# Kernel tuning notes

Measured on AMD Instinct MI355X. Metric: run time of the kernel, lower is better.

## Reference

```python
import jax, jax.numpy as jnp
import numpy as np

T, B, N = 1000, 64, 512
DT = 0.01
EL, VR, TR, TINF = -0.07, -0.07, -0.06, -0.05
A_VAL = 2.6239240169525146
A1_VAL = -0.015625353902578354
A2_VAL = -1.0590057373046875
B_VAL = 12.77495288848877
G_VAL = 45.24007797241211
K1, K2 = 200.0, 20.0
R1, R2 = 0.3858567178249359, -1.1421641111373901
C = 1.0


def setup_inputs() -> dict:
    key = jax.random.key(0)
    x = jax.random.normal(key, (T, B, N), dtype=jnp.float32)
    linear = jnp.ones((1, N), jnp.float32)
    a = jnp.full((1, N), A_VAL, jnp.float32)
    A1 = jnp.full((1, N), A1_VAL * C, jnp.float32)
    A2 = jnp.full((1, N), A2_VAL * C, jnp.float32)
    return {"x": x, "linear": linear, "a": a, "A1": A1, "A2": A2}


def _spike(v):
    # Heaviside step (forward of SurrGradSpike)
    return (v > 0).astype(v.dtype)


def reference(x, linear, a, A1, A2):
    G = G_VAL * C

    def step(state, xt):
        V, i1, i2, Thr = state
        i1 = i1 - K1 * i1 * DT
        i2 = i2 - K2 * i2 * DT
        V = V + DT * (linear * xt + i1 + i2 - G * (V - EL)) / C
        Thr = Thr + DT * (a * (V - EL) - B_VAL * (Thr - TINF))
        spk = _spike(V - Thr)
        i1 = (1.0 - spk) * i1 + spk * (R1 * i1 + A1)
        i2 = (1.0 - spk) * i2 + spk * (R2 * i2 + A2)
        Thr = (1.0 - spk) * Thr + spk * jnp.maximum(Thr, TR)
        V = (1.0 - spk) * V + spk * VR
        return (V, i1, i2, Thr), spk

    Bd, Nd = x.shape[1], x.shape[2]
    init = (
        jnp.full((Bd, Nd), EL, x.dtype),   # V
        jnp.zeros((Bd, Nd), x.dtype),      # i1
        jnp.zeros((Bd, Nd), x.dtype),      # i2
        jnp.full((Bd, Nd), TINF, x.dtype), # Thr
    )
    _, spikes = jax.lax.scan(step, init, x)
    return spikes  # [T, B, N] (original returns np.array of per-step spikes)
```

## Files before the change

kernel.cpp:

```cpp
#include <hip/hip_runtime.h>


#define T_STEPS 1000
#define B_DIM 64
#define N_DIM 512
#define BN (B_DIM * N_DIM)

#define K_CHUNK 20
#define NCHUNK (T_STEPS / K_CHUNK)
#define NBUF 8

#define C_DT   0.01f
#define C_EL   (-0.07f)
#define C_VR   (-0.07f)
#define C_TR   (-0.06f)
#define C_TINF (-0.05f)
#define C_B    12.77495288848877f
#define C_G    45.24007797241211f
#define C_K1   200.0f
#define C_K2   20.0f
#define C_R1   0.3858567178249359f
#define C_R2   (-1.1421641111373901f)

typedef const __attribute__((address_space(1))) void* gp_t;
typedef __attribute__((address_space(3))) void* lp_t;
typedef __attribute__((address_space(3))) float* lpf_t;

__device__ __forceinline__ float mn_step(float xt, float lin, float av,
                                         float A1v, float A2v,
                                         float& V, float& i1, float& i2,
                                         float& Thr)
{
#pragma clang fp contract(off)
    i1 = i1 - (C_K1 * i1) * C_DT;
    i2 = i2 - (C_K2 * i2) * C_DT;
    float p  = lin * xt;
    float q  = p + i1;
    float r  = q + i2;
    float e  = V - C_EL;
    float g  = C_G * e;
    float s  = r - g;
    float d  = C_DT * s;
    V = V + d;
    float e2 = V - C_EL;
    float u  = av * e2;
    float w  = Thr - C_TINF;
    float bw = C_B * w;
    float s2 = u - bw;
    float d2 = C_DT * s2;
    Thr = Thr + d2;
    float diff = V - Thr;
    bool  sb   = diff > 0.0f;
    float spk  = sb ? 1.0f : 0.0f;
    float i1r = (C_R1 * i1) + A1v;
    float i2r = (C_R2 * i2) + A2v;
    i1  = sb ? i1r : i1;
    i2  = sb ? i2r : i2;
    float tm = fmaxf(Thr, C_TR);
    Thr = sb ? tm : Thr;
    V   = sb ? C_VR : V;
    return spk;
}

__global__ __launch_bounds__(128) void mn_neuron_kernel(
    const float* __restrict__ x, const float* __restrict__ linear,
    const float* __restrict__ a, const float* __restrict__ A1,
    const float* __restrict__ A2, float* __restrict__ out)
{
#pragma clang fp contract(off)
    __shared__ float lds[NBUF][K_CHUNK][64];

    const int lane = threadIdx.x & 63;
    const int wid  = threadIdx.x >> 6;
    const int blk  = blockIdx.x;

    if (wid == 1) {
        const float* pl = x + (size_t)(lane >> 4) * BN
                            + (size_t)blk * 64 + (size_t)(lane & 15) * 4;

        auto issue_chunk = [&](int ch) {
            const float* pc = pl + (size_t)(ch * K_CHUNK) * BN;
            float* dst = &lds[ch & (NBUF - 1)][0][0];
#pragma unroll
            for (int s = 0; s < K_CHUNK / 4; ++s) {
                __builtin_amdgcn_global_load_lds(
                    (gp_t)(pc + (size_t)(s * 4) * BN),
                    (lp_t)(dst + s * 4 * 64), 16, 0, 0);
            }
        };

        for (int ch = 0; ch < NBUF - 1; ++ch) issue_chunk(ch);
        asm volatile("s_waitcnt vmcnt(30)" ::: "memory");
        __builtin_amdgcn_s_barrier();

        for (int c = 0; c <= NCHUNK - NBUF; ++c) {
            issue_chunk(c + NBUF - 1);
            asm volatile("s_waitcnt vmcnt(30)" ::: "memory");
            __builtin_amdgcn_s_barrier();
        }
        asm volatile("s_waitcnt vmcnt(25)" ::: "memory");
        __builtin_amdgcn_s_barrier();
        asm volatile("s_waitcnt vmcnt(20)" ::: "memory");
        __builtin_amdgcn_s_barrier();
        asm volatile("s_waitcnt vmcnt(15)" ::: "memory");
        __builtin_amdgcn_s_barrier();
        asm volatile("s_waitcnt vmcnt(10)" ::: "memory");
        __builtin_amdgcn_s_barrier();
        asm volatile("s_waitcnt vmcnt(5)" ::: "memory");
        __builtin_amdgcn_s_barrier();
        asm volatile("s_waitcnt vmcnt(0)" ::: "memory");
        __builtin_amdgcn_s_barrier();
        __builtin_amdgcn_s_barrier();
    } else {
        const int idx = blk * 64 + lane;
        const int n   = idx & (N_DIM - 1);

        const float lin = linear[n];
        const float av  = a[n];
        const float A1v = A1[n];
        const float A2v = A2[n];

        float V   = C_EL;
        float i1  = 0.0f;
        float i2  = 0.0f;
        float Thr = C_TINF;

        float* op = out + idx;

        __builtin_amdgcn_s_barrier();

        for (int c = 0; c < NCHUNK; ++c) {
            lpf_t lptr = (lpf_t)&lds[c & (NBUF - 1)][0][lane];

            float xv[K_CHUNK];
            asm volatile(
                "ds_read_b32 %0,  %20 offset:0\n\t"
                "ds_read_b32 %1,  %20 offset:256\n\t"
                "ds_read_b32 %2,  %20 offset:512\n\t"
                "ds_read_b32 %3,  %20 offset:768\n\t"
                "ds_read_b32 %4,  %20 offset:1024\n\t"
                "ds_read_b32 %5,  %20 offset:1280\n\t"
                "ds_read_b32 %6,  %20 offset:1536\n\t"
                "ds_read_b32 %7,  %20 offset:1792\n\t"
                "ds_read_b32 %8,  %20 offset:2048\n\t"
                "ds_read_b32 %9,  %20 offset:2304\n\t"
                "ds_read_b32 %10, %20 offset:2560\n\t"
                "ds_read_b32 %11, %20 offset:2816\n\t"
                "ds_read_b32 %12, %20 offset:3072\n\t"
                "ds_read_b32 %13, %20 offset:3328\n\t"
                "ds_read_b32 %14, %20 offset:3584\n\t"
                "ds_read_b32 %15, %20 offset:3840\n\t"
                "ds_read_b32 %16, %20 offset:4096\n\t"
                "ds_read_b32 %17, %20 offset:4352\n\t"
                "ds_read_b32 %18, %20 offset:4608\n\t"
                "ds_read_b32 %19, %20 offset:4864\n\t"
                "s_waitcnt lgkmcnt(0)"
                : "=&v"(xv[0]),  "=&v"(xv[1]),  "=&v"(xv[2]),  "=&v"(xv[3]),
                  "=&v"(xv[4]),  "=&v"(xv[5]),  "=&v"(xv[6]),  "=&v"(xv[7]),
                  "=&v"(xv[8]),  "=&v"(xv[9]),  "=&v"(xv[10]), "=&v"(xv[11]),
                  "=&v"(xv[12]), "=&v"(xv[13]), "=&v"(xv[14]), "=&v"(xv[15]),
                  "=&v"(xv[16]), "=&v"(xv[17]), "=&v"(xv[18]), "=&v"(xv[19])
                : "v"(lptr));

            __builtin_amdgcn_s_barrier();

#pragma unroll
            for (int j = 0; j < K_CHUNK; ++j) {
                float spk = mn_step(xv[j], lin, av, A1v, A2v, V, i1, i2, Thr);
                __builtin_nontemporal_store(spk, op);
                op += BN;
            }
        }
    }
}

extern "C" void kernel_launch(void* const* d_in, const int* in_sizes, int n_in,
                              void* d_out, int out_size, void* d_ws, size_t ws_size,
                              hipStream_t stream) {
    const float* x      = (const float*)d_in[0];
    const float* linear = (const float*)d_in[1];
    const float* a      = (const float*)d_in[2];
    const float* A1     = (const float*)d_in[3];
    const float* A2     = (const float*)d_in[4];
    float* out = (float*)d_out;

    mn_neuron_kernel<<<BN / 64, 128, 0, stream>>>(x, linear, a, A1, A2, out);
}
```

Baseline: 246.1 us.

## Speculatively precompute both spike branches to shorten per-step dependency chain

Restructures the neuron recurrence so that each step's reset-dependent quantities (i1/i2 decay, G*(V-EL), B*(Thr-TINF), clamped threshold) are computed for both the spike and no-spike outcomes ahead of time. The actual spike bit then only selects between the precomputed values. This is meant to take the reset selects and decay arithmetic off the serial critical path of the time loop, in exchange for extra ALU work and registers per step.

```diff
diff --git a/kernel.cpp b/kernel.cpp
--- a/kernel.cpp
+++ b/kernel.cpp
@@ -26,42 +26,6 @@
 typedef __attribute__((address_space(3))) void* lp_t;
 typedef __attribute__((address_space(3))) float* lpf_t;
 
-__device__ __forceinline__ float mn_step(float xt, float lin, float av,
-                                         float A1v, float A2v,
-                                         float& V, float& i1, float& i2,
-                                         float& Thr)
-{
-#pragma clang fp contract(off)
-    i1 = i1 - (C_K1 * i1) * C_DT;
-    i2 = i2 - (C_K2 * i2) * C_DT;
-    float p  = lin * xt;
-    float q  = p + i1;
-    float r  = q + i2;
-    float e  = V - C_EL;
-    float g  = C_G * e;
-    float s  = r - g;
-    float d  = C_DT * s;
-    V = V + d;
-    float e2 = V - C_EL;
-    float u  = av * e2;
-    float w  = Thr - C_TINF;
-    float bw = C_B * w;
-    float s2 = u - bw;
-    float d2 = C_DT * s2;
-    Thr = Thr + d2;
-    float diff = V - Thr;
-    bool  sb   = diff > 0.0f;
-    float spk  = sb ? 1.0f : 0.0f;
-    float i1r = (C_R1 * i1) + A1v;
-    float i2r = (C_R2 * i2) + A2v;
-    i1  = sb ? i1r : i1;
-    i2  = sb ? i2r : i2;
-    float tm = fmaxf(Thr, C_TR);
-    Thr = sb ? tm : Thr;
-    V   = sb ? C_VR : V;
-    return spk;
-}
-
 __global__ __launch_bounds__(128) void mn_neuron_kernel(
     const float* __restrict__ x, const float* __restrict__ linear,
     const float* __restrict__ a, const float* __restrict__ A1,
@@ -120,10 +84,15 @@
         const float A1v = A1[n];
         const float A2v = A2[n];
 
-        float V   = C_EL;
-        float i1  = 0.0f;
-        float i2  = 0.0f;
-        float Thr = C_TINF;
+        bool  sb   = false;
+        float V    = C_EL;
+        float Thr  = C_TINF;
+        float Thrm = C_TINF;
+        float P1 = 0.0f, Q1 = 0.0f, P2 = 0.0f, Q2 = 0.0f;
+        float sumP = 0.0f, sumQ = 0.0f;
+        float gA  = C_G * (C_EL - C_EL);
+        float bwA = C_B * (C_TINF - C_TINF);
+        float bwB = bwA;
 
         float* op = out + idx;
 
@@ -164,11 +133,54 @@
 
             __builtin_amdgcn_s_barrier();
 
+            {
+                float p0 = lin * xv[0];
+                sumP = (p0 + P1) + P2;
+                sumQ = (p0 + Q1) + Q2;
+            }
+
 #pragma unroll
             for (int j = 0; j < K_CHUNK; ++j) {
-                float spk = mn_step(xv[j], lin, av, A1v, A2v, V, i1, i2, Thr);
+                float r   = sb ? sumQ : sumP;
+                float gs  = sb ? 0.0f : gA;
+                float s   = r - gs;
+                float d   = C_DT * s;
+                float Vs  = sb ? C_VR : V;
+                float Vn  = Vs + d;
+                float e2  = Vn - C_EL;
+                float u   = av * e2;
+                float bws = sb ? bwB : bwA;
+                float s2  = u - bws;
+                float d2  = C_DT * s2;
+                float Ts  = sb ? Thrm : Thr;
+                float Tn  = Ts + d2;
+                float diff = Vn - Tn;
+                bool  sbn  = diff > 0.0f;
+
+                float spk = sbn ? 1.0f : 0.0f;
                 __builtin_nontemporal_store(spk, op);
                 op += BN;
+
+                float D1  = sb ? Q1 : P1;
+                float D2  = sb ? Q2 : P2;
+                float i1r = (C_R1 * D1) + A1v;
+                float i2r = (C_R2 * D2) + A2v;
+                P1 = D1  - (C_K1 * D1)  * C_DT;
+                Q1 = i1r - (C_K1 * i1r) * C_DT;
+                P2 = D2  - (C_K2 * D2)  * C_DT;
+                Q2 = i2r - (C_K2 * i2r) * C_DT;
+                if (j < K_CHUNK - 1) {
+                    float pn = lin * xv[j + 1];
+                    sumP = (pn + P1) + P2;
+                    sumQ = (pn + Q1) + Q2;
+                }
+                gA   = C_G * e2;
+                Thrm = fmaxf(Tn, C_TR);
+                float wA = Tn   - C_TINF;
+                float wB = Thrm - C_TINF;
+                bwA  = C_B * wA;
+                bwB  = C_B * wB;
+                V = Vn; Thr = Tn; sb = sbn;
             }
         }
     }
```

Result: no change. 247.8 us (+0.7%).
